# Kernel optimization log

Hardware: AMD Instinct MI355X
Metric: run time of the kernel (lower is better)

Reference implementation:

```python
import jax, jax.numpy as jnp
import numpy as np

B, T, D, H, HD = 128, 256, 512, 8, 64

def setup_inputs() -> dict:
    key = jax.random.key(0)
    ks = jax.random.split(key, 5)
    scale = 0.02
    return {
        "x": jax.random.normal(ks[0], (B, T, D), dtype=jnp.float32),
        "Wq": jax.random.normal(ks[1], (H, D, HD), dtype=jnp.float32) * scale,
        "Wk": jax.random.normal(ks[2], (H, D, HD), dtype=jnp.float32) * scale,
        "Wv": jax.random.normal(ks[3], (H, D, HD), dtype=jnp.float32) * scale,
        "Wo": jax.random.normal(ks[4], (D, D), dtype=jnp.float32) * scale,
        "bo": jnp.zeros((D,), dtype=jnp.float32),
    }

def reference(x, Wq, Wk, Wv, Wo, bo):
    # Per-head projections, batched over heads: [B,T,D] x [H,D,HD] -> [B,H,T,HD]
    q = jnp.einsum('btd,hdk->bhtk', x, Wq)
    k = jnp.einsum('btd,hdk->bhtk', x, Wk)
    v = jnp.einsum('btd,hdk->bhtk', x, Wv)
    # Scaled scores [B,H,T,T] with causal mask
    scores = jnp.einsum('bhtk,bhsk->bhts', q, k) * (HD ** -0.5)
    causal = jnp.tril(jnp.ones((T, T), dtype=bool))
    scores = jnp.where(causal, scores, jnp.finfo(scores.dtype).min)
    attn = jax.nn.softmax(scores, axis=-1)
    # Dropout is identity at inference.
    out = jnp.einsum('bhts,bhsk->bhtk', attn, v)
    # Concat heads: [B,T,H*HD] == [B,T,D]
    out = out.transpose(0, 2, 1, 3).reshape(B, T, D)
    # Output projection
    return out @ Wo + bo
```

## Files before the change

### kernel.cpp

```cpp
#include <hip/hip_runtime.h>
#include <hip/hip_bf16.h>

typedef __bf16 bf16x8 __attribute__((ext_vector_type(8)));
typedef __bf16 bf16x4 __attribute__((ext_vector_type(4)));
typedef float f32x4 __attribute__((ext_vector_type(4)));
typedef unsigned short u16x8 __attribute__((ext_vector_type(8)));


__device__ __forceinline__ unsigned short f2bf(float f) {
  unsigned u = __float_as_uint(f);
  u += 0x7fffu + ((u >> 16) & 1u);
  return (unsigned short)(u >> 16);
}

__device__ __forceinline__ bf16x4 cvt4(f32x4 v) {
  bf16x4 o;
  o[0] = (__bf16)v[0]; o[1] = (__bf16)v[1]; o[2] = (__bf16)v[2]; o[3] = (__bf16)v[3];
  return o;
}

__device__ __forceinline__ void async16(const void* g, void* l) {
  __builtin_amdgcn_global_load_lds(
      (const __attribute__((address_space(1))) void*)g,
      (__attribute__((address_space(3))) void*)l, 16, 0, 0);
}

__global__ __launch_bounds__(256) void k_convert_x(const float* __restrict__ in,
                                                   unsigned short* __restrict__ out) {
  int i = blockIdx.x * 256 + threadIdx.x;
  const float4* p = (const float4*)in + (size_t)i * 2;
  float4 a = p[0], b = p[1];
  u16x8 o;
  o[0] = f2bf(a.x); o[1] = f2bf(a.y); o[2] = f2bf(a.z); o[3] = f2bf(a.w);
  o[4] = f2bf(b.x); o[5] = f2bf(b.y); o[6] = f2bf(b.z); o[7] = f2bf(b.w);
  *((u16x8*)out + i) = o;
}

__global__ __launch_bounds__(256) void k_transpose_w(const float* __restrict__ in,
                                                     unsigned short* __restrict__ out,
                                                     int rows, int cols) {
  __shared__ unsigned short tile[64][72];
  int c0 = blockIdx.x * 64, r0 = blockIdx.y * 64;
  const float* inb = in + (size_t)blockIdx.z * rows * cols;
  unsigned short* outb = out + (size_t)blockIdx.z * rows * cols;
  int tid = threadIdx.x;
  int r = tid >> 2, cq = (tid & 3) * 16;
  const float* src = inb + (size_t)(r0 + r) * cols + c0 + cq;
#pragma unroll
  for (int i = 0; i < 16; i += 4) {
    float4 v = *(const float4*)(src + i);
    tile[r][cq + i + 0] = f2bf(v.x);
    tile[r][cq + i + 1] = f2bf(v.y);
    tile[r][cq + i + 2] = f2bf(v.z);
    tile[r][cq + i + 3] = f2bf(v.w);
  }
  __syncthreads();
  int cr = tid >> 2, rq = (tid & 3) * 16;
  u16x8 o0, o1;
#pragma unroll
  for (int i = 0; i < 8; ++i) o0[i] = tile[rq + i][cr];
#pragma unroll
  for (int i = 0; i < 8; ++i) o1[i] = tile[rq + 8 + i][cr];
  unsigned short* dst = outb + (size_t)(c0 + cr) * rows + r0 + rq;
  *(u16x8*)dst = o0;
  *(u16x8*)(dst + 8) = o1;
}

template <int KIND>
__global__ __launch_bounds__(512, 1) void k_gemmP(
    const unsigned short* __restrict__ A,
    const unsigned short* __restrict__ Bmat,
    unsigned short* __restrict__ O0,
    unsigned short* __restrict__ O1,
    const float* __restrict__ bo,
    float* __restrict__ outf) {
  __shared__ unsigned short smem[65536];
  const int P = (KIND == 0) ? 64 : 32;
  int xcd = blockIdx.x & 7, g = blockIdx.x >> 3;
  int w = xcd * P + g;
  int mt, nt;
  if (KIND == 0) { mt = w >> 2; nt = w & 3; }
  else           { mt = w >> 1; nt = w & 1; }
  int m0 = mt * 256, n0 = nt * 256;
  int tid = threadIdx.x;
  int wid = tid >> 6, lane = tid & 63;
  int lr = lane & 15, lg = lane >> 4;
  int wm = wid >> 2, wn = wid & 3;

  int srow = wid * 16 + (lane >> 3);
  int scs = (lane & 7) ^ (lane >> 3);
  auto stage_tile = [&](int kb, int buf) {
#pragma unroll
    for (int H = 0; H < 4; ++H) {
      const unsigned short* gb = (H < 2) ? (A + (size_t)(m0 + H * 128) * 512)
                                         : (Bmat + (size_t)(n0 + (H - 2) * 128) * 512);
#pragma unroll
      for (int j = 0; j < 2; ++j) {
        int row = srow + j * 8;
        async16(gb + (size_t)row * 512 + kb * 64 + scs * 8,
                smem + buf * 32768 + H * 8192 + (wid * 2 + j) * 512);
      }
    }
  };
  int xcol0 = ((0 * 64 + lg * 16) ^ ((lr & 7) * 16)) >> 1;
  int xcol1 = ((1 * 64 + lg * 16) ^ ((lr & 7) * 16)) >> 1;
  auto lda = [&](int buf, int mi, int k32) -> bf16x8 {
    int off = buf * 32768 + wm * 8192 + (mi * 16 + lr) * 64 + (k32 ? xcol1 : xcol0);
    return *(const bf16x8*)&smem[off];
  };
  auto ldb = [&](int buf, int ni, int k32) -> bf16x8 {
    int n = wn * 64 + ni * 16 + lr;
    int off = buf * 32768 + 16384 + (n >> 7) * 8192 + (n & 127) * 64 + (k32 ? xcol1 : xcol0);
    return *(const bf16x8*)&smem[off];
  };

  f32x4 acc[8][4];
#pragma unroll
  for (int mi = 0; mi < 8; ++mi)
#pragma unroll
    for (int ni = 0; ni < 4; ++ni) acc[mi][ni] = (f32x4){0.f, 0.f, 0.f, 0.f};

#define MF(dst, afrag, bfrag)                                                        \
  if constexpr (KIND == 2)                                                           \
    dst = __builtin_amdgcn_mfma_f32_16x16x32_bf16(afrag, bfrag, dst, 0, 0, 0);       \
  else                                                                               \
    dst = __builtin_amdgcn_mfma_f32_16x16x32_bf16(bfrag, afrag, dst, 0, 0, 0);

  stage_tile(0, 0);
  stage_tile(1, 1);
  asm volatile("s_waitcnt vmcnt(8)" ::: "memory");
  __builtin_amdgcn_s_barrier();
  asm volatile("" ::: "memory");

  bf16x8 a03[4][2], a47[4][2], b01[2][2], b23[2][2];
#pragma unroll
  for (int t = 0; t < 8; ++t) {
    int buf = t & 1;
#pragma unroll
    for (int mi = 0; mi < 4; ++mi) { a03[mi][0] = lda(buf, mi, 0); a03[mi][1] = lda(buf, mi, 1); }
#pragma unroll
    for (int ni = 0; ni < 2; ++ni) { b01[ni][0] = ldb(buf, ni, 0); b01[ni][1] = ldb(buf, ni, 1); }
    __builtin_amdgcn_s_setprio(1);
#pragma unroll
    for (int mi = 0; mi < 4; ++mi)
#pragma unroll
      for (int ni = 0; ni < 2; ++ni)
#pragma unroll
        for (int k = 0; k < 2; ++k) { MF(acc[mi][ni], a03[mi][k], b01[ni][k]); }
    __builtin_amdgcn_s_setprio(0);
    asm volatile("" ::: "memory");
    __builtin_amdgcn_s_barrier();
    asm volatile("" ::: "memory");
#pragma unroll
    for (int mi = 0; mi < 4; ++mi) { a47[mi][0] = lda(buf, mi + 4, 0); a47[mi][1] = lda(buf, mi + 4, 1); }
    __builtin_amdgcn_s_setprio(1);
#pragma unroll
    for (int mi = 0; mi < 4; ++mi)
#pragma unroll
      for (int ni = 0; ni < 2; ++ni)
#pragma unroll
        for (int k = 0; k < 2; ++k) { MF(acc[mi + 4][ni], a47[mi][k], b01[ni][k]); }
    __builtin_amdgcn_s_setprio(0);
    asm volatile("" ::: "memory");
    __builtin_amdgcn_s_barrier();
    asm volatile("" ::: "memory");
#pragma unroll
    for (int ni = 0; ni < 2; ++ni) { b23[ni][0] = ldb(buf, ni + 2, 0); b23[ni][1] = ldb(buf, ni + 2, 1); }
    __builtin_amdgcn_s_setprio(1);
#pragma unroll
    for (int mi = 0; mi < 4; ++mi)
#pragma unroll
      for (int ni = 0; ni < 2; ++ni)
#pragma unroll
        for (int k = 0; k < 2; ++k) { MF(acc[mi + 4][ni + 2], a47[mi][k], b23[ni][k]); }
    __builtin_amdgcn_s_setprio(0);
    asm volatile("" ::: "memory");
    __builtin_amdgcn_s_barrier();
    asm volatile("" ::: "memory");
    if (t < 6) stage_tile(t + 2, buf);
    __builtin_amdgcn_s_setprio(1);
#pragma unroll
    for (int mi = 0; mi < 4; ++mi)
#pragma unroll
      for (int ni = 0; ni < 2; ++ni)
#pragma unroll
        for (int k = 0; k < 2; ++k) { MF(acc[mi][ni + 2], a03[mi][k], b23[ni][k]); }
    __builtin_amdgcn_s_setprio(0);
    if (t < 6)       asm volatile("s_waitcnt vmcnt(8)" ::: "memory");
    else if (t == 6) asm volatile("s_waitcnt vmcnt(0)" ::: "memory");
    asm volatile("" ::: "memory");
    __builtin_amdgcn_s_barrier();
    asm volatile("" ::: "memory");
  }
#undef MF

  if constexpr (KIND == 0) {
    int z = n0 >> 9;
    int h = ((n0 + wn * 64) >> 6) & 7;
    unsigned short* outp = (z ? O1 : O0) + (size_t)(mt * 8 + h) * 16384;
#pragma unroll
    for (int ni = 0; ni < 4; ++ni) {
      int hd0 = ni * 16 + lg * 4;
#pragma unroll
      for (int mi = 0; mi < 8; ++mi) {
        int tq = wm * 128 + mi * 16 + lr;
        *(bf16x4*)&outp[(size_t)tq * 64 + hd0] = cvt4(acc[mi][ni]);
      }
    }
  } else if constexpr (KIND == 1) {
#pragma unroll
    for (int ni = 0; ni < 4; ++ni) {
      int nb = n0 + wn * 64 + ni * 16 + lg * 4;
      float4 b4 = *(const float4*)&bo[nb];
#pragma unroll
      for (int mi = 0; mi < 8; ++mi) {
        int mg = m0 + wm * 128 + mi * 16 + lr;
        float4 o;
        o.x = acc[mi][ni][0] + b4.x; o.y = acc[mi][ni][1] + b4.y;
        o.z = acc[mi][ni][2] + b4.z; o.w = acc[mi][ni][3] + b4.w;
        *(float4*)&outf[(size_t)mg * 512 + nb] = o;
      }
    }
  } else {
    int h = (n0 >> 6) + wn;
    unsigned short* outp = O0 + (size_t)(mt * 8 + h) * 16384;
#pragma unroll
    for (int ni = 0; ni < 4; ++ni) {
      int hd = ni * 16 + lr;
#pragma unroll
      for (int mi = 0; mi < 8; ++mi) {
        int tq = wm * 128 + mi * 16 + lg * 4;
        *(bf16x4*)&outp[(size_t)hd * 256 + tq] = cvt4(acc[mi][ni]);
      }
    }
  }
}

__global__ __launch_bounds__(512, 1) void k_attn2(
    const unsigned short* __restrict__ Qb,
    const unsigned short* __restrict__ Kb,
    const unsigned short* __restrict__ Vtb,
    unsigned short* __restrict__ Ob) {
  __shared__ unsigned short Ks[16384];
  __shared__ unsigned short Vs[16384];
  __shared__ unsigned short Ps[8][16][264];
  int bh = blockIdx.x;
  int tid = threadIdx.x, wid = tid >> 6, lane = tid & 63, lr = lane & 15, lg = lane >> 4;
  int bb = bh >> 3, h = bh & 7;
  const unsigned short* Kg = Kb + (size_t)bh * 16384;
  const unsigned short* Vg = Vtb + (size_t)bh * 16384;
#pragma unroll
  for (int c = 0; c < 4; ++c) {
    int d = (wid * 4 + c) * 64 + lane;
    int kr = d >> 3, kc = (d & 7) ^ (kr & 7);
    async16(Kg + (size_t)kr * 64 + kc * 8, Ks + (wid * 4 + c) * 512);
    int vr = d >> 5, vc = (d & 31) ^ ((vr & 7) << 2);
    async16(Vg + (size_t)vr * 256 + vc * 8, Vs + (wid * 4 + c) * 512);
  }
  __syncthreads();

#pragma unroll
  for (int cc = 0; cc < 2; ++cc) {
    int ci = cc ? (15 - wid) : wid;
    int t0 = ci * 16, trow = t0 + lr;
    int ntV = ci + 1;
    int ntE = (ntV + 1) & ~1;
    int nk32 = ntE >> 1;
    const unsigned short* qsrc = Qb + (size_t)bh * 16384 + (size_t)(t0 + lr) * 64 + lg * 8;
    bf16x8 bq0 = *(const bf16x8*)qsrc;
    bf16x8 bq1 = *(const bf16x8*)(qsrc + 32);
    f32x4 acc[16];
#pragma unroll
    for (int nt = 0; nt < 16; ++nt)
      if (nt < ntE) acc[nt] = (f32x4){0.f, 0.f, 0.f, 0.f};
#pragma unroll
    for (int nt = 0; nt < 16; ++nt)
      if (nt < ntV) {
        int row = nt * 16 + lr;
        bf16x8 ak0 = *(const bf16x8*)&Ks[row * 64 + ((0 + lg) ^ (lr & 7)) * 8];
        acc[nt] = __builtin_amdgcn_mfma_f32_16x16x32_bf16(ak0, bq0, acc[nt], 0, 0, 0);
        bf16x8 ak1 = *(const bf16x8*)&Ks[row * 64 + ((4 + lg) ^ (lr & 7)) * 8];
        acc[nt] = __builtin_amdgcn_mfma_f32_16x16x32_bf16(ak1, bq1, acc[nt], 0, 0, 0);
      }
    float m = -3.0e38f;
#pragma unroll
    for (int nt = 0; nt < 16; ++nt)
      if (nt < ntE) {
#pragma unroll
        for (int r = 0; r < 4; ++r) {
          float v = acc[nt][r] * 0.125f;
          if (nt * 16 + lg * 4 + r > trow) v = -1.0e30f;
          acc[nt][r] = v;
          m = fmaxf(m, v);
        }
      }
    m = fmaxf(m, __shfl_xor(m, 16));
    m = fmaxf(m, __shfl_xor(m, 32));
    float s = 0.f;
#pragma unroll
    for (int nt = 0; nt < 16; ++nt)
      if (nt < ntE) {
        bf16x4 pk;
#pragma unroll
        for (int r = 0; r < 4; ++r) {
          float p = __expf(acc[nt][r] - m);
          s += p;
          pk[r] = (__bf16)p;
        }
        *(bf16x4*)&Ps[wid][lr][nt * 16 + lg * 4] = pk;
      }
    s += __shfl_xor(s, 16);
    s += __shfl_xor(s, 32);
    float inv = 1.0f / s;
    __threadfence_block();
    f32x4 aco[4];
#pragma unroll
    for (int vt = 0; vt < 4; ++vt) aco[vt] = (f32x4){0.f, 0.f, 0.f, 0.f};
#pragma unroll
    for (int k32 = 0; k32 < 8; ++k32)
      if (k32 < nk32) {
        bf16x8 pb = *(const bf16x8*)&Ps[wid][lr][k32 * 32 + lg * 8];
#pragma unroll
        for (int vt = 0; vt < 4; ++vt) {
          int row = vt * 16 + lr;
          bf16x8 av = *(const bf16x8*)&Vs[row * 256 + (((k32 * 4 + lg) ^ ((lr & 7) << 2)) * 8)];
          aco[vt] = __builtin_amdgcn_mfma_f32_16x16x32_bf16(av, pb, aco[vt], 0, 0, 0);
        }
      }
    unsigned short* obase = Ob + (size_t)(bb * 256 + trow) * 512 + h * 64 + lg * 4;
#pragma unroll
    for (int vt = 0; vt < 4; ++vt) {
      bf16x4 ov;
#pragma unroll
      for (int r = 0; r < 4; ++r) ov[r] = (__bf16)(aco[vt][r] * inv);
      *(bf16x4*)(obase + vt * 16) = ov;
    }
    __threadfence_block();
  }
}

extern "C" void kernel_launch(void* const* d_in, const int* in_sizes, int n_in,
                              void* d_out, int out_size, void* d_ws, size_t ws_size,
                              hipStream_t stream) {
  (void)in_sizes; (void)n_in; (void)out_size; (void)ws_size;
  const float* x = (const float*)d_in[0];
  const float* Wq = (const float*)d_in[1];
  const float* Wk = (const float*)d_in[2];
  const float* Wv = (const float*)d_in[3];
  const float* Wo = (const float*)d_in[4];
  const float* bo = (const float*)d_in[5];
  float* out = (float*)d_out;
  char* ws = (char*)d_ws;
  const size_t MB = 1024 * 1024;
  unsigned short* Qb = (unsigned short*)(ws);
  unsigned short* Kb = (unsigned short*)(ws + 32 * MB);
  unsigned short* Vtb = (unsigned short*)(ws + 64 * MB);
  unsigned short* xb = (unsigned short*)(ws + 96 * MB);
  unsigned short* Wqt = (unsigned short*)(ws + 128 * MB);
  unsigned short* Wkt = Wqt + 262144;
  unsigned short* Wvt = Wkt + 262144;
  unsigned short* Wot = Wvt + 262144;

  hipLaunchKernelGGL(k_convert_x, dim3(8192), dim3(256), 0, stream, x, xb);
  hipLaunchKernelGGL(k_transpose_w, dim3(1, 8, 8), dim3(256), 0, stream, Wq, Wqt, 512, 64);
  hipLaunchKernelGGL(k_transpose_w, dim3(1, 8, 8), dim3(256), 0, stream, Wk, Wkt, 512, 64);
  hipLaunchKernelGGL(k_transpose_w, dim3(1, 8, 8), dim3(256), 0, stream, Wv, Wvt, 512, 64);
  hipLaunchKernelGGL(k_transpose_w, dim3(8, 8, 1), dim3(256), 0, stream, Wo, Wot, 512, 512);
  hipLaunchKernelGGL((k_gemmP<0>), dim3(512), dim3(512), 0, stream,
                     xb, Wqt, Qb, Kb, (const float*)nullptr, (float*)nullptr);
  hipLaunchKernelGGL((k_gemmP<2>), dim3(256), dim3(512), 0, stream,
                     xb, Wvt, Vtb, (unsigned short*)nullptr, (const float*)nullptr, (float*)nullptr);
  hipLaunchKernelGGL(k_attn2, dim3(1024), dim3(512), 0, stream, Qb, Kb, Vtb, xb);
  hipLaunchKernelGGL((k_gemmP<1>), dim3(256), dim3(512), 0, stream,
                     xb, Wot, (unsigned short*)nullptr, (unsigned short*)nullptr, bo, out);
}
```

Measured before the change: 176.6 us.

## Merge QKV weight transposes into one launch and cut GEMM inner-loop barriers

The three per-head weight transpose launches are merged into one kernel that picks Wq/Wk/Wv from blockIdx.z, which saves two kernel launches. In the GEMM main loop, all A and B fragments for a k-tile are now loaded from LDS up front. This cuts the loop from four barriers to two, and the MFMAs then run in two larger batches. The cost is higher register pressure from holding every fragment live, and less overlap between LDS reads and MFMA work.

```diff
diff --git a/kernel.cpp b/kernel.cpp
--- a/kernel.cpp
+++ b/kernel.cpp
@@ -36,16 +36,19 @@
   *((u16x8*)out + i) = o;
 }
 
-__global__ __launch_bounds__(256) void k_transpose_w(const float* __restrict__ in,
-                                                     unsigned short* __restrict__ out,
-                                                     int rows, int cols) {
+__global__ __launch_bounds__(256) void k_transpose_w3(const float* __restrict__ w0,
+                                                      const float* __restrict__ w1,
+                                                      const float* __restrict__ w2,
+                                                      unsigned short* __restrict__ out) {
   __shared__ unsigned short tile[64][72];
-  int c0 = blockIdx.x * 64, r0 = blockIdx.y * 64;
-  const float* inb = in + (size_t)blockIdx.z * rows * cols;
-  unsigned short* outb = out + (size_t)blockIdx.z * rows * cols;
+  int z = blockIdx.z;
+  int wsel = z >> 3, hsel = z & 7;
+  const float* inb = (wsel == 0 ? w0 : (wsel == 1 ? w1 : w2)) + (size_t)hsel * 512 * 64;
+  unsigned short* outb = out + (size_t)z * 512 * 64;
+  int r0 = blockIdx.y * 64;
   int tid = threadIdx.x;
   int r = tid >> 2, cq = (tid & 3) * 16;
-  const float* src = inb + (size_t)(r0 + r) * cols + c0 + cq;
+  const float* src = inb + (size_t)(r0 + r) * 64 + cq;
 #pragma unroll
   for (int i = 0; i < 16; i += 4) {
     float4 v = *(const float4*)(src + i);
@@ -61,7 +64,35 @@
   for (int i = 0; i < 8; ++i) o0[i] = tile[rq + i][cr];
 #pragma unroll
   for (int i = 0; i < 8; ++i) o1[i] = tile[rq + 8 + i][cr];
-  unsigned short* dst = outb + (size_t)(c0 + cr) * rows + r0 + rq;
+  unsigned short* dst = outb + (size_t)cr * 512 + r0 + rq;
+  *(u16x8*)dst = o0;
+  *(u16x8*)(dst + 8) = o1;
+}
+
+__global__ __launch_bounds__(256) void k_transpose_w(const float* __restrict__ in,
+                                                     unsigned short* __restrict__ out,
+                                                     int rows, int cols) {
+  __shared__ unsigned short tile[64][72];
+  int c0 = blockIdx.x * 64, r0 = blockIdx.y * 64;
+  int tid = threadIdx.x;
+  int r = tid >> 2, cq = (tid & 3) * 16;
+  const float* src = in + (size_t)(r0 + r) * cols + c0 + cq;
+#pragma unroll
+  for (int i = 0; i < 16; i += 4) {
+    float4 v = *(const float4*)(src + i);
+    tile[r][cq + i + 0] = f2bf(v.x);
+    tile[r][cq + i + 1] = f2bf(v.y);
+    tile[r][cq + i + 2] = f2bf(v.z);
+    tile[r][cq + i + 3] = f2bf(v.w);
+  }
+  __syncthreads();
+  int cr = tid >> 2, rq = (tid & 3) * 16;
+  u16x8 o0, o1;
+#pragma unroll
+  for (int i = 0; i < 8; ++i) o0[i] = tile[rq + i][cr];
+#pragma unroll
+  for (int i = 0; i < 8; ++i) o1[i] = tile[rq + 8 + i][cr];
+  unsigned short* dst = out + (size_t)(c0 + cr) * rows + r0 + rq;
   *(u16x8*)dst = o0;
   *(u16x8*)(dst + 8) = o1;
 }
@@ -137,9 +168,15 @@
   for (int t = 0; t < 8; ++t) {
     int buf = t & 1;
 #pragma unroll
-    for (int mi = 0; mi < 4; ++mi) { a03[mi][0] = lda(buf, mi, 0); a03[mi][1] = lda(buf, mi, 1); }
-#pragma unroll
-    for (int ni = 0; ni < 2; ++ni) { b01[ni][0] = ldb(buf, ni, 0); b01[ni][1] = ldb(buf, ni, 1); }
+    for (int mi = 0; mi < 4; ++mi) {
+      a03[mi][0] = lda(buf, mi, 0);     a03[mi][1] = lda(buf, mi, 1);
+      a47[mi][0] = lda(buf, mi + 4, 0); a47[mi][1] = lda(buf, mi + 4, 1);
+    }
+#pragma unroll
+    for (int ni = 0; ni < 2; ++ni) {
+      b01[ni][0] = ldb(buf, ni, 0);     b01[ni][1] = ldb(buf, ni, 1);
+      b23[ni][0] = ldb(buf, ni + 2, 0); b23[ni][1] = ldb(buf, ni + 2, 1);
+    }
     __builtin_amdgcn_s_setprio(1);
 #pragma unroll
     for (int mi = 0; mi < 4; ++mi)
@@ -147,13 +184,6 @@
       for (int ni = 0; ni < 2; ++ni)
 #pragma unroll
         for (int k = 0; k < 2; ++k) { MF(acc[mi][ni], a03[mi][k], b01[ni][k]); }
-    __builtin_amdgcn_s_setprio(0);
-    asm volatile("" ::: "memory");
-    __builtin_amdgcn_s_barrier();
-    asm volatile("" ::: "memory");
-#pragma unroll
-    for (int mi = 0; mi < 4; ++mi) { a47[mi][0] = lda(buf, mi + 4, 0); a47[mi][1] = lda(buf, mi + 4, 1); }
-    __builtin_amdgcn_s_setprio(1);
 #pragma unroll
     for (int mi = 0; mi < 4; ++mi)
 #pragma unroll
@@ -161,20 +191,7 @@
 #pragma unroll
         for (int k = 0; k < 2; ++k) { MF(acc[mi + 4][ni], a47[mi][k], b01[ni][k]); }
     __builtin_amdgcn_s_setprio(0);
-    asm volatile("" ::: "memory");
-    __builtin_amdgcn_s_barrier();
-    asm volatile("" ::: "memory");
-#pragma unroll
-    for (int ni = 0; ni < 2; ++ni) { b23[ni][0] = ldb(buf, ni + 2, 0); b23[ni][1] = ldb(buf, ni + 2, 1); }
-    __builtin_amdgcn_s_setprio(1);
-#pragma unroll
-    for (int mi = 0; mi < 4; ++mi)
-#pragma unroll
-      for (int ni = 0; ni < 2; ++ni)
-#pragma unroll
-        for (int k = 0; k < 2; ++k) { MF(acc[mi + 4][ni + 2], a47[mi][k], b23[ni][k]); }
-    __builtin_amdgcn_s_setprio(0);
-    asm volatile("" ::: "memory");
+    asm volatile("s_waitcnt lgkmcnt(0)" ::: "memory");
     __builtin_amdgcn_s_barrier();
     asm volatile("" ::: "memory");
     if (t < 6) stage_tile(t + 2, buf);
@@ -185,6 +202,12 @@
       for (int ni = 0; ni < 2; ++ni)
 #pragma unroll
         for (int k = 0; k < 2; ++k) { MF(acc[mi][ni + 2], a03[mi][k], b23[ni][k]); }
+#pragma unroll
+    for (int mi = 0; mi < 4; ++mi)
+#pragma unroll
+      for (int ni = 0; ni < 2; ++ni)
+#pragma unroll
+        for (int k = 0; k < 2; ++k) { MF(acc[mi + 4][ni + 2], a47[mi][k], b23[ni][k]); }
     __builtin_amdgcn_s_setprio(0);
     if (t < 6)       asm volatile("s_waitcnt vmcnt(8)" ::: "memory");
     else if (t == 6) asm volatile("s_waitcnt vmcnt(0)" ::: "memory");
@@ -362,9 +385,7 @@
   unsigned short* Wot = Wvt + 262144;
 
   hipLaunchKernelGGL(k_convert_x, dim3(8192), dim3(256), 0, stream, x, xb);
-  hipLaunchKernelGGL(k_transpose_w, dim3(1, 8, 8), dim3(256), 0, stream, Wq, Wqt, 512, 64);
-  hipLaunchKernelGGL(k_transpose_w, dim3(1, 8, 8), dim3(256), 0, stream, Wk, Wkt, 512, 64);
-  hipLaunchKernelGGL(k_transpose_w, dim3(1, 8, 8), dim3(256), 0, stream, Wv, Wvt, 512, 64);
+  hipLaunchKernelGGL(k_transpose_w3, dim3(1, 8, 24), dim3(256), 0, stream, Wq, Wk, Wv, Wqt);
   hipLaunchKernelGGL(k_transpose_w, dim3(8, 8, 1), dim3(256), 0, stream, Wo, Wot, 512, 512);
   hipLaunchKernelGGL((k_gemmP<0>), dim3(512), dim3(512), 0, stream,
                      xb, Wqt, Qb, Kb, (const float*)nullptr, (float*)nullptr);
```

Result: slower. 184.0 us (+4.2%).
